# Kernel optimization log

Measured on AMD Instinct MI355X. Metric: run time of the kernel, lower is better.

Reference implementation:

```python
import jax, jax.numpy as jnp
import numpy as np

N_NODES = 100000
N_EDGES = 1600000
D = 128


def setup_inputs() -> dict:
    key = jax.random.key(0)
    ks = jax.random.split(key, 8)
    x = jax.random.normal(ks[0], (N_NODES, D), dtype=jnp.float32)
    edge_index = jax.random.randint(ks[1], (2, N_EDGES), 0, N_NODES, dtype=jnp.int64)
    # Linear weights ~ fan-in scaled init
    scale = 1.0 / np.sqrt(D)
    W1 = jax.random.normal(ks[2], (D, D), dtype=jnp.float32) * scale
    W2 = jax.random.normal(ks[3], (D, D), dtype=jnp.float32) * scale
    W3 = jax.random.normal(ks[4], (D, D), dtype=jnp.float32) * scale
    b1 = jnp.zeros((D,), jnp.float32)
    b2 = jnp.zeros((D,), jnp.float32)
    b3 = jnp.zeros((D,), jnp.float32)
    # train_eps=True, PyG initializes eps to 0
    eps1 = jnp.zeros((), jnp.float32)
    eps2 = jnp.zeros((), jnp.float32)
    eps3 = jnp.zeros((), jnp.float32)
    return {"x": x, "edge_index": edge_index,
            "W1": W1, "b1": b1, "eps1": eps1,
            "W2": W2, "b2": b2, "eps2": eps2,
            "W3": W3, "b3": b3, "eps3": eps3}


def _gin_conv(x, src, dst, eps, W, b):
    # scatter-add neighbor aggregation: sum_{j in N(i)} x_j
    agg = jax.ops.segment_sum(x[src], dst, num_segments=N_NODES)  # [N, D]
    h = (1.0 + eps) * x + agg
    return jax.nn.relu(h @ W + b)


def reference(x, edge_index, W1, b1, eps1, W2, b2, eps2, W3, b3, eps3):
    src, dst = edge_index[0], edge_index[1]
    h = _gin_conv(x, src, dst, eps1, W1, b1)   # conv1 (dropout p=0 -> identity)
    h = _gin_conv(h, src, dst, eps2, W2, b2)
    h = _gin_conv(h, src, dst, eps3, W3, b3)
    return jax.nn.log_softmax(h, axis=1)
```

## Files before the change

kernel.cpp:

```cpp
#include <hip/hip_runtime.h>
#include <hip/hip_bf16.h>

#define N_NODES 100000
#define N_EDGES 1600000
#define D 128
#define NRANGE 8
#define RANGE_SZ 12500
#define SB_PER_RANGE 196
#define NBUCKET (NRANGE * SB_PER_RANGE)
#define G_PART 512
#define CH_PART 3125
#define G_DEG 128
#define CH_DEG 784
#define G_X2B 12500

typedef __attribute__((ext_vector_type(8))) short bf16x8;
typedef __attribute__((ext_vector_type(8))) unsigned short u16x8;
typedef __attribute__((ext_vector_type(4))) float f32x4;
typedef unsigned int u32;

__device__ inline ushort f2b(float x) {
    union { float f; unsigned u; } v; v.f = x;
    unsigned r = (v.u + 0x7fff + ((v.u >> 16) & 1)) >> 16;
    return (ushort)r;
}
__device__ inline float b2f(ushort b) {
    union { unsigned u; float f; } v; v.u = ((unsigned)b) << 16;
    return v.f;
}

__global__ void prep_kernel(const float* __restrict__ x, ushort* __restrict__ xb,
                            const int* __restrict__ dst, int* __restrict__ bhist1,
                            const float* __restrict__ W1, const float* __restrict__ W2,
                            const float* __restrict__ W3,
                            ushort* __restrict__ wt_hi, ushort* __restrict__ wt_lo) {
    __shared__ int lh[NRANGE];
    int b = blockIdx.x;
    if (b < G_X2B) {
        int i = b * 256 + threadIdx.x;
        if (i < N_NODES * D / 4) {
            float4 v = ((const float4*)x)[i];
            ushort4 o;
            o.x = f2b(v.x); o.y = f2b(v.y); o.z = f2b(v.z); o.w = f2b(v.w);
            ((ushort4*)xb)[i] = o;
        }
    } else if (b < G_X2B + G_PART) {
        int blk = b - G_X2B;
        if (threadIdx.x < NRANGE) lh[threadIdx.x] = 0;
        __syncthreads();
        int s0 = blk * CH_PART, s1 = s0 + CH_PART;
        if (s1 > N_EDGES) s1 = N_EDGES;
        for (int i = s0 + threadIdx.x; i < s1; i += 256)
            atomicAdd(&lh[dst[i] / RANGE_SZ], 1);
        __syncthreads();
        if (threadIdx.x < NRANGE) bhist1[blk * NRANGE + threadIdx.x] = lh[threadIdx.x];
    } else {
        int blk = b - G_X2B - G_PART;
        int layer = blk >> 6;
        int t = (blk & 63) * 256 + threadIdx.x;
        const float* W = layer == 0 ? W1 : layer == 1 ? W2 : W3;
        int k = t >> 7, n = t & 127;
        float w = W[t];
        ushort hi = f2b(w);
        ushort lo = f2b(w - b2f(hi));
        wt_hi[layer * D * D + n * D + k] = hi;
        wt_lo[layer * D * D + n * D + k] = lo;
    }
}


__global__ void scan1_kernel(const int* __restrict__ bhist1, int* __restrict__ cbase1,
                             int* __restrict__ rs) {
    int r = threadIdx.x >> 6, lane = threadIdx.x & 63;
    __shared__ int rtot[NRANGE], roff[NRANGE];
    int excl[8];
    int run = 0;
    #pragma unroll
    for (int seg = 0; seg < 8; ++seg) {
        int b = seg * 64 + lane;
        int v = bhist1[b * NRANGE + r];
        int sc = v;
        #pragma unroll
        for (int off = 1; off < 64; off <<= 1) {
            int y = __shfl_up(sc, off);
            if (lane >= off) sc += y;
        }
        excl[seg] = run + sc - v;
        run += __shfl(sc, 63);
    }
    if (lane == 63) rtot[r] = run;
    __syncthreads();
    if (threadIdx.x == 0) {
        int a = 0;
        for (int i = 0; i < NRANGE; ++i) { roff[i] = a; a += rtot[i]; }
    }
    __syncthreads();
    int base = roff[r];
    #pragma unroll
    for (int seg = 0; seg < 8; ++seg)
        cbase1[(seg * 64 + lane) * NRANGE + r] = base + excl[seg];
    if (threadIdx.x < NRANGE) rs[threadIdx.x] = roff[threadIdx.x];
    if (threadIdx.x == 0) rs[NRANGE] = N_EDGES;
}

__global__ void place1_kernel(const int* __restrict__ src, const int* __restrict__ dst,
                              const int* __restrict__ cbase1, u32* __restrict__ epack1) {
    __shared__ int cur[NRANGE];
    if (threadIdx.x < NRANGE) cur[threadIdx.x] = cbase1[blockIdx.x * NRANGE + threadIdx.x];
    __syncthreads();
    int s0 = blockIdx.x * CH_PART, s1 = s0 + CH_PART;
    if (s1 > N_EDGES) s1 = N_EDGES;
    for (int i = s0 + threadIdx.x; i < s1; i += 256) {
        int d = dst[i], s = src[i];
        int r = d / RANGE_SZ;
        int dl = d - r * RANGE_SZ;
        int p = atomicAdd(&cur[r], 1);
        epack1[p] = ((u32)dl << 17) | (u32)s;
    }
}

__global__ void hist2_kernel(const u32* __restrict__ epack1, const int* __restrict__ rs,
                             int* __restrict__ bhist2) {
    __shared__ int lh[SB_PER_RANGE];
    for (int i = threadIdx.x; i < SB_PER_RANGE; i += 256) lh[i] = 0;
    __syncthreads();
    int r = blockIdx.x >> 6, j = blockIdx.x & 63;
    int e0 = rs[r], e1 = rs[r + 1];
    int cs = (e1 - e0 + 63) >> 6;
    int s0 = e0 + j * cs, s1 = s0 + cs;
    if (s1 > e1) s1 = e1;
    for (int i = s0 + threadIdx.x; i < s1; i += 256)
        atomicAdd(&lh[epack1[i] >> 23], 1);
    __syncthreads();
    for (int i = threadIdx.x; i < SB_PER_RANGE; i += 256)
        bhist2[blockIdx.x * SB_PER_RANGE + i] = lh[i];
}

__global__ void scan2_kernel(const int* __restrict__ bhist2, const int* __restrict__ rs,
                             int* __restrict__ cbase2, int* __restrict__ bucket_start) {
    int r = blockIdx.x;
    __shared__ int tot[SB_PER_RANGE];
    __shared__ int base[SB_PER_RANGE];
    int sb = threadIdx.x;
    if (sb < SB_PER_RANGE) {
        int s = 0;
        for (int j = 0; j < 64; ++j) s += bhist2[(r * 64 + j) * SB_PER_RANGE + sb];
        tot[sb] = s;
    }
    __syncthreads();
    if (threadIdx.x == 0) {
        int a = 0;
        for (int i = 0; i < SB_PER_RANGE; ++i) { base[i] = a; a += tot[i]; }
    }
    __syncthreads();
    if (sb < SB_PER_RANGE) {
        int run = rs[r] + base[sb];
        bucket_start[r * SB_PER_RANGE + sb] = run;
        for (int j = 0; j < 64; ++j) {
            cbase2[(r * 64 + j) * SB_PER_RANGE + sb] = run;
            run += bhist2[(r * 64 + j) * SB_PER_RANGE + sb];
        }
    }
    if (r == NRANGE - 1 && threadIdx.x == 0) bucket_start[NBUCKET] = N_EDGES;
}

__global__ void place2_kernel(const u32* __restrict__ epack1, const int* __restrict__ rs,
                              const int* __restrict__ cbase2, u32* __restrict__ epack2) {
    __shared__ int cur[SB_PER_RANGE];
    for (int i = threadIdx.x; i < SB_PER_RANGE; i += 256)
        cur[i] = cbase2[blockIdx.x * SB_PER_RANGE + i];
    __syncthreads();
    int r = blockIdx.x >> 6, j = blockIdx.x & 63;
    int e0 = rs[r], e1 = rs[r + 1];
    int cs = (e1 - e0 + 63) >> 6;
    int s0 = e0 + j * cs, s1 = s0 + cs;
    if (s1 > e1) s1 = e1;
    for (int i = s0 + threadIdx.x; i < s1; i += 256) {
        u32 e = epack1[i];
        int sb = e >> 23;
        int p = atomicAdd(&cur[sb], 1);
        epack2[p] = e & 0x7FFFFFu;
    }
}

__global__ void sort3_kernel(const u32* __restrict__ epack2, const int* __restrict__ bucket_start,
                             int* __restrict__ row_ptr, int* __restrict__ col,
                             int* __restrict__ deg) {
    int b = blockIdx.x;
    int r = b / SB_PER_RANGE, sb = b - r * SB_PER_RANGE;
    int node_base = r * RANGE_SZ + sb * 64;
    int nb = r * RANGE_SZ + RANGE_SZ - node_base;
    if (nb > 64) nb = 64;
    int e0 = bucket_start[b], e1 = bucket_start[b + 1];
    __shared__ int hist[64], cur[64];
    if (threadIdx.x < 64) hist[threadIdx.x] = 0;
    __syncthreads();
    for (int i = e0 + threadIdx.x; i < e1; i += 256)
        atomicAdd(&hist[(epack2[i] >> 17) & 63], 1);
    __syncthreads();
    if (threadIdx.x < 64) {
        int v = hist[threadIdx.x];
        int sc = v;
        #pragma unroll
        for (int off = 1; off < 64; off <<= 1) {
            int y = __shfl_up(sc, off);
            if (threadIdx.x >= off) sc += y;
        }
        int ex = e0 + sc - v;
        cur[threadIdx.x] = ex;
        if (threadIdx.x < nb) {
            row_ptr[node_base + threadIdx.x] = ex;
            deg[node_base + threadIdx.x] = v;
        }
    }
    __syncthreads();
    for (int i = e0 + threadIdx.x; i < e1; i += 256) {
        u32 e = epack2[i];
        int l = (e >> 17) & 63;
        int p = atomicAdd(&cur[l], 1);
        col[p] = (int)(e & 0x1FFFFu);
    }
    if (b == NBUCKET - 1 && threadIdx.x == 0) row_ptr[N_NODES] = N_EDGES;
}


__global__ void deghist_kernel(const int* __restrict__ deg, int* __restrict__ bdh) {
    __shared__ int lh[128];
    if (threadIdx.x < 128) lh[threadIdx.x] = 0;
    __syncthreads();
    int s0 = blockIdx.x * CH_DEG, s1 = s0 + CH_DEG;
    if (s1 > N_NODES) s1 = N_NODES;
    for (int i = s0 + threadIdx.x; i < s1; i += 256)
        atomicAdd(&lh[min(deg[i], 127)], 1);
    __syncthreads();
    if (threadIdx.x < 128) bdh[blockIdx.x * 128 + threadIdx.x] = lh[threadIdx.x];
}

__global__ void degscan_kernel(const int* __restrict__ bdh, int* __restrict__ cbdeg) {
    __shared__ int sh[128];
    int t = threadIdx.x;
    int tot = 0;
    for (int j = 0; j < G_DEG; ++j) tot += bdh[j * 128 + t];
    sh[t] = tot;
    __syncthreads();
    if (t == 0) {
        int run = 0;
        for (int b = 127; b >= 0; --b) { int c = sh[b]; sh[b] = run; run += c; }
    }
    __syncthreads();
    int run = sh[t];
    for (int j = 0; j < G_DEG; ++j) {
        cbdeg[j * 128 + t] = run;
        run += bdh[j * 128 + t];
    }
}

__global__ void degplace_kernel(const int* __restrict__ deg, const int* __restrict__ cbdeg,
                                int* __restrict__ perm) {
    __shared__ int cur[128];
    if (threadIdx.x < 128) cur[threadIdx.x] = cbdeg[blockIdx.x * 128 + threadIdx.x];
    __syncthreads();
    int s0 = blockIdx.x * CH_DEG, s1 = s0 + CH_DEG;
    if (s1 > N_NODES) s1 = N_NODES;
    for (int i = s0 + threadIdx.x; i < s1; i += 256) {
        int p = atomicAdd(&cur[min(deg[i], 127)], 1);
        perm[p] = i;
    }
}


__global__ void aggregate_kernel(const ushort* __restrict__ xb, const int* __restrict__ row_ptr,
                                 const int* __restrict__ col, const int* __restrict__ perm,
                                 const float* __restrict__ eps_p, ushort* __restrict__ hb) {
    int q = (blockIdx.x * blockDim.x + threadIdx.x) >> 4;
    if (q >= N_NODES) return;
    int node = perm[q];
    int l16 = threadIdx.x & 15;
    int beg = row_ptr[node], end = row_ptr[node + 1];
    float a0[8] = {0,0,0,0,0,0,0,0};
    float a1[8] = {0,0,0,0,0,0,0,0};
    int e = beg;
    for (; e + 7 < end; e += 8) {
        int s[8];
        #pragma unroll
        for (int j = 0; j < 8; ++j) s[j] = col[e + j];
        u16x8 v[8];
        #pragma unroll
        for (int j = 0; j < 8; ++j)
            v[j] = *(const u16x8*)(xb + ((size_t)s[j] << 7) + l16 * 8);
        #pragma unroll
        for (int j = 0; j < 8; ++j) {
            float* a = (j & 1) ? a1 : a0;
            #pragma unroll
            for (int k = 0; k < 8; ++k) a[k] += b2f(v[j][k]);
        }
    }
    if (e + 3 < end) {
        int s[4];
        #pragma unroll
        for (int j = 0; j < 4; ++j) s[j] = col[e + j];
        u16x8 v[4];
        #pragma unroll
        for (int j = 0; j < 4; ++j)
            v[j] = *(const u16x8*)(xb + ((size_t)s[j] << 7) + l16 * 8);
        #pragma unroll
        for (int j = 0; j < 4; ++j) {
            float* a = (j & 1) ? a1 : a0;
            #pragma unroll
            for (int k = 0; k < 8; ++k) a[k] += b2f(v[j][k]);
        }
        e += 4;
    }
    for (; e < end; ++e) {
        int s = col[e];
        u16x8 v = *(const u16x8*)(xb + ((size_t)s << 7) + l16 * 8);
        #pragma unroll
        for (int k = 0; k < 8; ++k) a0[k] += b2f(v[k]);
    }
    float scale = 1.0f + *eps_p;
    u16x8 xi = *(const u16x8*)(xb + ((size_t)node << 7) + l16 * 8);
    u16x8 ho;
    #pragma unroll
    for (int k = 0; k < 8; ++k) {
        float o = a0[k] + a1[k] + scale * b2f(xi[k]);
        ho[k] = f2b(o);
    }
    *(u16x8*)(hb + ((size_t)node << 7) + l16 * 8) = ho;
}

template <int MODE>
__launch_bounds__(256, 2)
__global__ void gemm_relu_mfma(const ushort* __restrict__ hb,
                               const ushort* __restrict__ wt_hi, const ushort* __restrict__ wt_lo,
                               const float* __restrict__ bias,
                               float* __restrict__ outf, ushort* __restrict__ outb) {
    int wv = threadIdx.x >> 6, lane = threadIdx.x & 63;
    int r0 = blockIdx.x * 128 + wv * 32;
    int arow = lane & 15, agrp = lane >> 4;
    bf16x8 Ah[2][4];
    #pragma unroll
    for (int mf = 0; mf < 2; ++mf) {
        size_t rbase = (size_t)(r0 + mf * 16 + arow) * D;
        #pragma unroll
        for (int kf = 0; kf < 4; ++kf)
            Ah[mf][kf] = *(const bf16x8*)(hb + rbase + kf * 32 + agrp * 8);
    }
    f32x4 acc[2][8];
    #pragma unroll
    for (int mf = 0; mf < 2; ++mf)
        #pragma unroll
        for (int nf = 0; nf < 8; ++nf)
            acc[mf][nf] = (f32x4){0.f, 0.f, 0.f, 0.f};
    #pragma unroll
    for (int nf = 0; nf < 8; ++nf) {
        #pragma unroll
        for (int kf = 0; kf < 4; ++kf) {
            size_t wb = (size_t)(nf * 16 + arow) * D + kf * 32 + agrp * 8;
            bf16x8 bh = *(const bf16x8*)(wt_hi + wb);
            bf16x8 bl = *(const bf16x8*)(wt_lo + wb);
            #pragma unroll
            for (int mf = 0; mf < 2; ++mf) {
                acc[mf][nf] = __builtin_amdgcn_mfma_f32_16x16x32_bf16(Ah[mf][kf], bh, acc[mf][nf], 0, 0, 0);
                acc[mf][nf] = __builtin_amdgcn_mfma_f32_16x16x32_bf16(Ah[mf][kf], bl, acc[mf][nf], 0, 0, 0);
            }
        }
    }
    float bcol[8];
    #pragma unroll
    for (int nf = 0; nf < 8; ++nf) bcol[nf] = bias[nf * 16 + arow];
    if (MODE == 0) {
        int crow = agrp * 4;
        #pragma unroll
        for (int mf = 0; mf < 2; ++mf) {
            #pragma unroll
            for (int nf = 0; nf < 8; ++nf) {
                int coln = nf * 16 + arow;
                #pragma unroll
                for (int r = 0; r < 4; ++r) {
                    int row = r0 + mf * 16 + crow + r;
                    if (row < N_NODES)
                        outb[(size_t)row * D + coln] = f2b(fmaxf(acc[mf][nf][r] + bcol[nf], 0.f));
                }
            }
        }
    } else {
        #pragma unroll
        for (int mf = 0; mf < 2; ++mf) {
            #pragma unroll
            for (int rr = 0; rr < 4; ++rr) {
                float v[8];
                #pragma unroll
                for (int nf = 0; nf < 8; ++nf)
                    v[nf] = fmaxf(acc[mf][nf][rr] + bcol[nf], 0.f);
                float m = v[0];
                #pragma unroll
                for (int nf = 1; nf < 8; ++nf) m = fmaxf(m, v[nf]);
                #pragma unroll
                for (int off = 1; off < 16; off <<= 1) m = fmaxf(m, __shfl_xor(m, off));
                float s = 0.f;
                #pragma unroll
                for (int nf = 0; nf < 8; ++nf) s += __expf(v[nf] - m);
                #pragma unroll
                for (int off = 1; off < 16; off <<= 1) s += __shfl_xor(s, off);
                float lse = m + __logf(s);
                int row = r0 + mf * 16 + agrp * 4 + rr;
                if (row < N_NODES) {
                    #pragma unroll
                    for (int nf = 0; nf < 8; ++nf)
                        outf[(size_t)row * D + nf * 16 + arow] = v[nf] - lse;
                }
            }
        }
    }
}

extern "C" void kernel_launch(void* const* d_in, const int* in_sizes, int n_in,
                              void* d_out, int out_size, void* d_ws, size_t ws_size,
                              hipStream_t stream) {
    (void)in_sizes; (void)n_in; (void)out_size; (void)ws_size;
    const float* x  = (const float*)d_in[0];
    const int*   ei = (const int*)d_in[1];
    const int*   src = ei;
    const int*   dst = ei + N_EDGES;
    const float* W1 = (const float*)d_in[2];
    const float* b1 = (const float*)d_in[3];
    const float* e1 = (const float*)d_in[4];
    const float* W2 = (const float*)d_in[5];
    const float* b2 = (const float*)d_in[6];
    const float* e2 = (const float*)d_in[7];
    const float* W3 = (const float*)d_in[8];
    const float* b3 = (const float*)d_in[9];
    const float* e3 = (const float*)d_in[10];
    float* out = (float*)d_out;

    char* ws = (char*)d_ws;
    int*    rs           = (int*)ws;
    int*    bucket_start = (int*)(ws + 1024);
    int*    bhist1       = (int*)(ws + 8192);
    int*    cbase1       = (int*)(ws + 24576);
    int*    bhist2       = (int*)(ws + 40960);
    int*    cbase2       = (int*)(ws + 442368);
    int*    row_ptr      = (int*)(ws + 851968);
    int*    deg          = (int*)(ws + 1253376);
    int*    perm         = (int*)(ws + 1654784);
    int*    bdh          = (int*)(ws + 2055168);
    int*    cbdeg        = (int*)(ws + 2120704);
    int*    col          = (int*)(ws + 2193408);
    ushort* wt_hi        = (ushort*)(ws + 8650752);
    ushort* wt_lo        = (ushort*)(ws + 8749056);
    ushort* xb           = (ushort*)(ws + 9437184);
    ushort* hb           = (ushort*)(ws + 35651584);
    u32*    epack1       = (u32*)(ws + 35651584);
    u32*    epack2       = (u32*)(ws + 42991616);

    prep_kernel<<<G_X2B + G_PART + 192, 256, 0, stream>>>(x, xb, dst, bhist1,
                                                          W1, W2, W3, wt_hi, wt_lo);

    scan1_kernel<<<1, 512, 0, stream>>>(bhist1, cbase1, rs);
    place1_kernel<<<G_PART, 256, 0, stream>>>(src, dst, cbase1, epack1);
    hist2_kernel<<<G_PART, 256, 0, stream>>>(epack1, rs, bhist2);
    scan2_kernel<<<NRANGE, 256, 0, stream>>>(bhist2, rs, cbase2, bucket_start);
    place2_kernel<<<G_PART, 256, 0, stream>>>(epack1, rs, cbase2, epack2);
    sort3_kernel<<<NBUCKET, 256, 0, stream>>>(epack2, bucket_start, row_ptr, col, deg);

    deghist_kernel<<<G_DEG, 256, 0, stream>>>(deg, bdh);
    degscan_kernel<<<1, 128, 0, stream>>>(bdh, cbdeg);
    degplace_kernel<<<G_DEG, 256, 0, stream>>>(deg, cbdeg, perm);

    const int aggGrid = (N_NODES * 16 + 255) / 256;
    const int gemmGrid = (N_NODES + 127) / 128;

    aggregate_kernel<<<aggGrid, 256, 0, stream>>>(xb, row_ptr, col, perm, e1, hb);
    gemm_relu_mfma<0><<<gemmGrid, 256, 0, stream>>>(hb, wt_hi, wt_lo, b1, nullptr, xb);
    aggregate_kernel<<<aggGrid, 256, 0, stream>>>(xb, row_ptr, col, perm, e2, hb);
    gemm_relu_mfma<0><<<gemmGrid, 256, 0, stream>>>(hb, wt_hi + D * D, wt_lo + D * D, b2, nullptr, xb);
    aggregate_kernel<<<aggGrid, 256, 0, stream>>>(xb, row_ptr, col, perm, e3, hb);
    gemm_relu_mfma<1><<<gemmGrid, 256, 0, stream>>>(hb, wt_hi + 2 * D * D, wt_lo + 2 * D * D, b3, out, nullptr);
}
```

Measured before the change: 381.0 us.

## Split bf16 feature storage into two 64-column planes for aggregation locality

```diff
diff --git a/kernel.cpp b/kernel.cpp
--- a/kernel.cpp
+++ b/kernel.cpp
@@ -13,6 +13,7 @@
 #define G_DEG 128
 #define CH_DEG 784
 #define G_X2B 12500
+#define PLANE ((size_t)N_NODES * 64)
 
 typedef __attribute__((ext_vector_type(8))) short bf16x8;
 typedef __attribute__((ext_vector_type(8))) unsigned short u16x8;
@@ -42,7 +43,10 @@
             float4 v = ((const float4*)x)[i];
             ushort4 o;
             o.x = f2b(v.x); o.y = f2b(v.y); o.z = f2b(v.z); o.w = f2b(v.w);
-            ((ushort4*)xb)[i] = o;
+            int node = i >> 5;
+            int f0 = (i & 31) * 4;
+            int plane = f0 >> 6;
+            *(ushort4*)(xb + plane * PLANE + (size_t)node * 64 + (f0 & 63)) = o;
         }
     } else if (b < G_X2B + G_PART) {
         int blk = b - G_X2B;
@@ -272,10 +276,13 @@
 __global__ void aggregate_kernel(const ushort* __restrict__ xb, const int* __restrict__ row_ptr,
                                  const int* __restrict__ col, const int* __restrict__ perm,
                                  const float* __restrict__ eps_p, ushort* __restrict__ hb) {
-    int q = (blockIdx.x * blockDim.x + threadIdx.x) >> 4;
-    if (q >= N_NODES) return;
-    int node = perm[q];
-    int l16 = threadIdx.x & 15;
+    int plane = blockIdx.x & 1;
+    int task = threadIdx.x >> 3;
+    int l8 = threadIdx.x & 7;
+    int qidx = (blockIdx.x >> 1) * 32 + task;
+    if (qidx >= N_NODES) return;
+    int node = perm[qidx];
+    const ushort* xp = xb + plane * PLANE;
     int beg = row_ptr[node], end = row_ptr[node + 1];
     float a0[8] = {0,0,0,0,0,0,0,0};
     float a1[8] = {0,0,0,0,0,0,0,0};
@@ -287,7 +294,7 @@
         u16x8 v[8];
         #pragma unroll
         for (int j = 0; j < 8; ++j)
-            v[j] = *(const u16x8*)(xb + ((size_t)s[j] << 7) + l16 * 8);
+            v[j] = *(const u16x8*)(xp + ((size_t)s[j] << 6) + l8 * 8);
         #pragma unroll
         for (int j = 0; j < 8; ++j) {
             float* a = (j & 1) ? a1 : a0;
@@ -302,7 +309,7 @@
         u16x8 v[4];
         #pragma unroll
         for (int j = 0; j < 4; ++j)
-            v[j] = *(const u16x8*)(xb + ((size_t)s[j] << 7) + l16 * 8);
+            v[j] = *(const u16x8*)(xp + ((size_t)s[j] << 6) + l8 * 8);
         #pragma unroll
         for (int j = 0; j < 4; ++j) {
             float* a = (j & 1) ? a1 : a0;
@@ -313,19 +320,19 @@
     }
     for (; e < end; ++e) {
         int s = col[e];
-        u16x8 v = *(const u16x8*)(xb + ((size_t)s << 7) + l16 * 8);
+        u16x8 v = *(const u16x8*)(xp + ((size_t)s << 6) + l8 * 8);
         #pragma unroll
         for (int k = 0; k < 8; ++k) a0[k] += b2f(v[k]);
     }
     float scale = 1.0f + *eps_p;
-    u16x8 xi = *(const u16x8*)(xb + ((size_t)node << 7) + l16 * 8);
+    u16x8 xi = *(const u16x8*)(xp + ((size_t)node << 6) + l8 * 8);
     u16x8 ho;
     #pragma unroll
     for (int k = 0; k < 8; ++k) {
         float o = a0[k] + a1[k] + scale * b2f(xi[k]);
         ho[k] = f2b(o);
     }
-    *(u16x8*)(hb + ((size_t)node << 7) + l16 * 8) = ho;
+    *(u16x8*)(hb + plane * PLANE + ((size_t)node << 6) + l8 * 8) = ho;
 }
 
 template <int MODE>
@@ -340,10 +347,14 @@
     bf16x8 Ah[2][4];
     #pragma unroll
     for (int mf = 0; mf < 2; ++mf) {
-        size_t rbase = (size_t)(r0 + mf * 16 + arow) * D;
-        #pragma unroll
-        for (int kf = 0; kf < 4; ++kf)
-            Ah[mf][kf] = *(const bf16x8*)(hb + rbase + kf * 32 + agrp * 8);
+        int row = r0 + mf * 16 + arow;
+        size_t rb0 = (size_t)row << 6;
+        #pragma unroll
+        for (int kf = 0; kf < 4; ++kf) {
+            size_t off = (kf < 2) ? rb0 + kf * 32 + agrp * 8
+                                  : PLANE + rb0 + (kf - 2) * 32 + agrp * 8;
+            Ah[mf][kf] = *(const bf16x8*)(hb + off);
+        }
     }
     f32x4 acc[2][8];
     #pragma unroll
@@ -375,11 +386,13 @@
             #pragma unroll
             for (int nf = 0; nf < 8; ++nf) {
                 int coln = nf * 16 + arow;
+                size_t pbase = (nf >> 2) ? PLANE : 0;
                 #pragma unroll
                 for (int r = 0; r < 4; ++r) {
                     int row = r0 + mf * 16 + crow + r;
                     if (row < N_NODES)
-                        outb[(size_t)row * D + coln] = f2b(fmaxf(acc[mf][nf][r] + bcol[nf], 0.f));
+                        outb[pbase + ((size_t)row << 6) + (coln & 63)] =
+                            f2b(fmaxf(acc[mf][nf][r] + bcol[nf], 0.f));
                 }
             }
         }
@@ -467,7 +480,7 @@
     degscan_kernel<<<1, 128, 0, stream>>>(bdh, cbdeg);
     degplace_kernel<<<G_DEG, 256, 0, stream>>>(deg, cbdeg, perm);
 
-    const int aggGrid = (N_NODES * 16 + 255) / 256;
+    const int aggGrid = 2 * ((N_NODES + 31) / 32);
     const int gemmGrid = (N_NODES + 127) / 128;
 
     aggregate_kernel<<<aggGrid, 256, 0, stream>>>(xb, row_ptr, col, perm, e1, hb);
```

After: 371.1 us (median of 2 runs). 2.6% less time.
